# Performance work log

Hardware: AMD Instinct MI355X
Metric: run time of the kernel (lower is better)

## Reference

```python
import jax, jax.numpy as jnp
import numpy as np

HEAD = 8

def setup_inputs() -> dict:
    key = jax.random.key(0)
    ks = jax.random.split(key, 11)
    B, C, W, H = 16, 512, 32, 32
    d, N = C // HEAD, W * H
    return {
        "x": jax.random.normal(ks[0], (B, C, W, H), jnp.float32),
        "Wq": jax.random.normal(ks[1], (C, C), jnp.float32) * 0.02,
        "bq": jax.random.normal(ks[2], (C,), jnp.float32) * 0.02,
        "Wk": jax.random.normal(ks[3], (C, C), jnp.float32) * 0.02,
        "bk": jax.random.normal(ks[4], (C,), jnp.float32) * 0.02,
        "Wv": jax.random.normal(ks[5], (C, C), jnp.float32) * 0.02,
        "bv": jax.random.normal(ks[6], (C,), jnp.float32) * 0.02,
        "rel_h": jax.random.normal(ks[7], (1, HEAD, d, 1, H), jnp.float32),
        "rel_w": jax.random.normal(ks[8], (1, HEAD, d, W, 1), jnp.float32),
        "reg_qk": jax.random.normal(ks[9], (1, N, N), jnp.float32),
        "reg_v": jax.random.normal(ks[10], (1, d, N), jnp.float32),
    }

def reference(x, Wq, bq, Wk, bk, Wv, bv, rel_h, rel_w, reg_qk, reg_v):
    B, C, W, H = x.shape
    head = HEAD
    d = C // head
    N = W * H
    def conv1x1(inp, Wt, b):  # 1x1 conv == per-pixel linear
        return jnp.einsum('bchw,oc->bohw', inp, Wt) + b[None, :, None, None]
    q = conv1x1(x, Wq, bq).reshape(B, head, d, N)
    k = conv1x1(x, Wk, bk).reshape(B, head, d, N)
    v = conv1x1(x, Wv, bv).reshape(B, head, d, N)
    # content-content: q^T k -> [B, head, N, N]
    cc = jnp.einsum('bhdn,bhdm->bhnm', q, k)
    # content-position: (rel_h + rel_w) broadcast to [1, head, d, W, H] -> [head, N, d]
    pos = (rel_h + rel_w).reshape(head, d, N)
    cp = jnp.einsum('hdn,bhdm->bhnm', pos, q)
    energy = cc + cp  # [B, head, N, N]
    n_reg = reg_qk.shape[0]
    energy = jnp.concatenate(
        [energy, jnp.broadcast_to(reg_qk[None], (B, n_reg, N, N))], axis=1)
    v_all = jnp.concatenate(
        [v, jnp.broadcast_to(reg_v[None], (B, n_reg, d, N))], axis=1)
    attn = jax.nn.softmax(energy, axis=-1)  # [B, head+n_reg, N, N]
    # v @ attn^T
    out = jnp.einsum('bgdn,bgmn->bgdm', v_all, attn)
    out = out[:, :head].reshape(B, C, W, H)
    return out + x
```

## Files before the change

### kernel.cpp

```cpp
#include <hip/hip_runtime.h>

#define BB   16
#define HEADS 8
#define DH   64
#define NSP  1024
#define CCH  512

typedef unsigned int   u32;
typedef unsigned short u16;
typedef __attribute__((ext_vector_type(8))) short  short8;
typedef __attribute__((ext_vector_type(4))) float  floatx4;
typedef __attribute__((ext_vector_type(2))) unsigned uint2v;

#if defined(__has_builtin)
#if __has_builtin(__builtin_amdgcn_exp2f)
#define EXP2F(x) __builtin_amdgcn_exp2f(x)
#else
#define EXP2F(x) exp2f(x)
#endif
#if __has_builtin(__builtin_amdgcn_permlane32_swap)
#define HAVE_PL32 1
#endif
#if __has_builtin(__builtin_amdgcn_permlane16_swap)
#define HAVE_PL16 1
#endif
#else
#define EXP2F(x) exp2f(x)
#endif

__device__ __forceinline__ u16 f2b(float f) {
  u32 x = __float_as_uint(f);
  x = x + 0x7fffu + ((x >> 16) & 1u);
  return (u16)(x >> 16);
}

__device__ __forceinline__ u32 pkbf(float lo, float hi) {
  return __builtin_amdgcn_perm(__float_as_uint(hi) + 0x8000u,
                               __float_as_uint(lo) + 0x8000u, 0x07060302u);
}

__device__ __forceinline__ u32 pkcvt(float lo, float hi) {
  u32 d;
  asm("v_cvt_pk_bf16_f32 %0, %1, %2" : "=v"(d) : "v"(lo), "v"(hi));
  return d;
}

__device__ __forceinline__ void gload_lds16(const u16* g, u16* l) {
  __builtin_amdgcn_global_load_lds((const __attribute__((address_space(1))) u32*)g,
                                   (__attribute__((address_space(3))) u32*)l, 16, 0, 0);
}

__device__ __forceinline__ void lane32_swap(u32 a, u32 b, u32& ap, u32& bp, bool hi32) {
#ifdef HAVE_PL32
  uint2v r = __builtin_amdgcn_permlane32_swap(a, b, false, false);
  ap = r.x; bp = r.y;
  (void)hi32;
#else
  u32 sb = (u32)__shfl_xor((int)b, 32);
  u32 sa = (u32)__shfl_xor((int)a, 32);
  ap = hi32 ? sb : a;
  bp = hi32 ? b : sa;
#endif
}

__device__ __forceinline__ u32 lane16_xor(u32 x, bool qodd) {
#ifdef HAVE_PL16
  uint2v r = __builtin_amdgcn_permlane16_swap(x, x, false, false);
  return qodd ? r.x : r.y;
#else
  return (u32)__shfl_xor((int)x, 16);
#endif
}


__global__ __launch_bounds__(256) void prep_all(const float* __restrict__ x,
                                                const float* __restrict__ Wq,
                                                const float* __restrict__ Wk,
                                                const float* __restrict__ Wv,
                                                const float* __restrict__ rel_h,
                                                const float* __restrict__ rel_w,
                                                u16* __restrict__ wbf,
                                                u16* __restrict__ pos,
                                                u16* __restrict__ xt) {
  __shared__ float ld[64][68];
  int bid = blockIdx.x;
  int t = threadIdx.x;
  if (bid < 768) {
    int idx = bid * 256 + t;
    int which = idx >> 16;
    int r4 = (idx & 65535) * 4;
    const float* src = which == 0 ? Wq : which == 1 ? Wk : Wv;
    float4 v = *(const float4*)&src[r4];
    ushort4 s;
    s.x = f2b(v.x); s.y = f2b(v.y); s.z = f2b(v.z); s.w = f2b(v.w);
    *(ushort4*)&wbf[(which << 18) + r4] = s;
  } else if (bid < 2816) {
    int idx = (bid - 768) * 256 + t;
    int dd = idx & 63;
    int n  = (idx >> 6) & 1023;
    int hd = idx >> 16;
    int ww = n >> 5, hh = n & 31;
    float v = rel_h[(hd * 64 + dd) * 32 + hh] + rel_w[(hd * 64 + dd) * 32 + ww];
    int ntp = n >> 6, nbp = (n >> 4) & 3, rp = n & 15;
    int ksp = dd >> 5, qp = (dd >> 3) & 3, ep = dd & 7;
    size_t off = ((((size_t)(hd * 16 + ntp) * 4 + nbp) * 2 + ksp) * 64 + qp * 16 + rp) * 8 + ep;
    pos[off] = f2b(v);
  } else {
    int bid2 = bid - 2816;
    int ntile = bid2 & 15, ctile = (bid2 >> 4) & 7, b = bid2 >> 7;
    const float* xb = x + (((size_t)b * CCH + ctile * 64) << 10) + ntile * 64;
#pragma unroll
    for (int p = 0; p < 4; ++p) {
      int c = p * 16 + (t >> 4), n4 = (t & 15) * 4;
      float4 v = *(const float4*)&xb[((size_t)c << 10) + n4];
      ld[c][n4 + 0] = v.x; ld[c][n4 + 1] = v.y; ld[c][n4 + 2] = v.z; ld[c][n4 + 3] = v.w;
    }
    __syncthreads();
    u16* xo = xt + (((size_t)b << 10) + ntile * 64) * CCH + ctile * 64;
#pragma unroll
    for (int p = 0; p < 2; ++p) {
      int id = p * 256 + t;
      int n = id >> 3, c8 = (id & 7) * 8;
      ushort4 s0, s1;
      s0.x = f2b(ld[c8 + 0][n]); s0.y = f2b(ld[c8 + 1][n]);
      s0.z = f2b(ld[c8 + 2][n]); s0.w = f2b(ld[c8 + 3][n]);
      s1.x = f2b(ld[c8 + 4][n]); s1.y = f2b(ld[c8 + 5][n]);
      s1.z = f2b(ld[c8 + 6][n]); s1.w = f2b(ld[c8 + 7][n]);
      *(ushort4*)&xo[(size_t)n * CCH + c8] = s0;
      *(ushort4*)&xo[(size_t)n * CCH + c8 + 4] = s1;
    }
  }
}

__global__ __launch_bounds__(256, 2) void qkv_fused(const u16* __restrict__ wbf,
                                                    const u16* __restrict__ xt,
                                                    const float* __restrict__ bq,
                                                    const float* __restrict__ bk,
                                                    const float* __restrict__ bv,
                                                    u16* __restrict__ qw,
                                                    u16* __restrict__ kw,
                                                    u16* __restrict__ vtw) {
  int hid = blockIdx.x;
  int xcd  = hid & 7;
  int slot = hid >> 3;
  int otile = slot & 7;
  int pair  = xcd * 16 + (slot >> 3);
  int ntile = pair & 7;
  int b     = pair >> 3;
  int o0 = otile * 64, n0 = ntile * 128;

  __shared__ __align__(16) u16 smem[2 * 20480];

  int t = threadIdx.x;
  int w = t >> 6, lane = t & 63;
  int l15 = lane & 15, quad = lane >> 4;
  int srow = lane >> 3, sc = lane & 7;
  int scc = (sc ^ srow) << 3;

  floatx4 aq[8], ak[8], av[8];
#pragma unroll
  for (int i = 0; i < 8; ++i) {
    aq[i] = (floatx4){0.f, 0.f, 0.f, 0.f};
    ak[i] = (floatx4){0.f, 0.f, 0.f, 0.f};
    av[i] = (floatx4){0.f, 0.f, 0.f, 0.f};
  }

  auto stage = [&](int k0, int buf) {
    u16* base = smem + buf * 20480;
#pragma unroll
    for (int p = 0; p < 10; ++p) {
      int g0 = w * 80 + p * 8;
      if (g0 < 192) {
        int which = g0 >> 6;
        int r0 = g0 & 63;
        gload_lds16(wbf + ((size_t)which << 18) + (size_t)(o0 + r0 + srow) * CCH + k0 + scc,
                    base + which * 4096 + r0 * 64);
      } else {
        int r0 = g0 - 192;
        gload_lds16(xt + (size_t)(b * 1024 + n0 + r0 + srow) * CCH + k0 + scc,
                    base + 12288 + r0 * 64);
      }
    }
  };

  int rs = l15 & 7;
  int c0 = (quad ^ rs) << 3;
  int c1 = ((4 + quad) ^ rs) << 3;
  int wrow = (w * 16 + l15) * 64;

  stage(0, 0);
  stage(64, 1);

  for (int ki = 0; ki < 8; ++ki) {
    if (ki < 7) asm volatile("s_waitcnt vmcnt(10)" ::: "memory");
    else        asm volatile("s_waitcnt vmcnt(0)" ::: "memory");
    __builtin_amdgcn_s_barrier();
    __builtin_amdgcn_sched_barrier(0);

    u16* base = smem + (ki & 1) * 20480;
    u16* Xb = base + 12288;
#pragma unroll
    for (int ks = 0; ks < 2; ++ks) {
      int cc = ks ? c1 : c0;
      short8 fq = *(short8*)&base[wrow + cc];
      short8 fk = *(short8*)&base[4096 + wrow + cc];
      short8 fv = *(short8*)&base[8192 + wrow + cc];
#pragma unroll
      for (int ns = 0; ns < 8; ++ns) {
        short8 fx = *(short8*)&Xb[(ns * 16 + l15) * 64 + cc];
        aq[ns] = __builtin_amdgcn_mfma_f32_16x16x32_bf16(fq, fx, aq[ns], 0, 0, 0);
        ak[ns] = __builtin_amdgcn_mfma_f32_16x16x32_bf16(fk, fx, ak[ns], 0, 0, 0);
        av[ns] = __builtin_amdgcn_mfma_f32_16x16x32_bf16(fx, fv, av[ns], 0, 0, 0);
      }
    }

    if (ki < 6) {
      __builtin_amdgcn_sched_barrier(0);
      __builtin_amdgcn_s_barrier();
      stage((ki + 2) * 64, ki & 1);
    }
  }

  __syncthreads();
  u16* epQ = smem;
  u16* epK = smem + 9216;
  u16* epV = smem + 18432;
  {
    int ob = o0 + w * 16 + quad * 4;
    float q0 = bq[ob], q1 = bq[ob + 1], q2 = bq[ob + 2], q3 = bq[ob + 3];
    float k0b = bk[ob], k1b = bk[ob + 1], k2b = bk[ob + 2], k3b = bk[ob + 3];
    float vb = bv[o0 + w * 16 + l15];
#pragma unroll
    for (int ns = 0; ns < 8; ++ns) {
      int n = ns * 16 + l15;
      uint2 pk;
      pk.x = pkbf(aq[ns][0] + q0, aq[ns][1] + q1);
      pk.y = pkbf(aq[ns][2] + q2, aq[ns][3] + q3);
      *(uint2*)&epQ[n * 72 + w * 16 + quad * 4] = pk;
      pk.x = pkbf(ak[ns][0] + k0b, ak[ns][1] + k1b);
      pk.y = pkbf(ak[ns][2] + k2b, ak[ns][3] + k3b);
      *(uint2*)&epK[n * 72 + w * 16 + quad * 4] = pk;
      pk.x = pkbf(av[ns][0] + vb, av[ns][1] + vb);
      pk.y = pkbf(av[ns][2] + vb, av[ns][3] + vb);
      *(uint2*)&epV[(w * 16 + l15) * 136 + ns * 16 + quad * 4] = pk;
    }
  }
  __syncthreads();
  int h = otile;
  size_t bhI = (size_t)(b * HEADS + h);
  {
    int row = t >> 1, half = t & 1;
    int nt_ = (n0 + row) >> 6;
    int nblk_ = (row >> 4) & 3;
    int r_ = row & 15;
    size_t qkbase = (((bhI * 16 + nt_) * 4 + nblk_) * 2 + half) * 512;
#pragma unroll
    for (int i = 0; i < 4; ++i)
      *(uint4*)&qw[qkbase + (i * 16 + r_) * 8] = *(uint4*)&epQ[row * 72 + half * 32 + i * 8];
#pragma unroll
    for (int i = 0; i < 4; ++i)
      *(uint4*)&kw[qkbase + (i * 16 + r_) * 8] = *(uint4*)&epK[row * 72 + half * 32 + i * 8];
  }
  {
    int row = t >> 2, q4 = t & 3;
    int ddblk = row >> 4, r_ = row & 15;
#pragma unroll
    for (int i = 0; i < 4; ++i) {
      int nl = q4 * 32 + i * 8;
      int n = n0 + nl;
      int ntv = n >> 6, np = n & 63;
      int nh = np >> 5, q = (np >> 3) & 3;
      size_t vbase = (((bhI * 16 + ntv) * 4 + ddblk) * 2 + nh) * 512;
      *(uint4*)&vtw[vbase + (q * 16 + r_) * 8] = *(uint4*)&epV[row * 136 + nl];
    }
  }
}

__global__ __launch_bounds__(256, 2) void attn_mfma(const u16* __restrict__ qw,
                                                    const u16* __restrict__ kw,
                                                    const u16* __restrict__ vtw,
                                                    const u16* __restrict__ pos,
                                                    const float* __restrict__ x,
                                                    float* __restrict__ out) {
  int bh = blockIdx.x, mtile = blockIdx.y;
  int b = bh >> 3, h = bh & 7;
  __shared__ __align__(16) u16 smem_u16[36864];

  int t = threadIdx.x;
  int w = t >> 6, lane = t & 63;
  int l15 = lane & 15, quad = lane >> 4;
  bool qodd = (quad & 1) != 0;
  bool hi32 = lane >= 32;
  size_t bhs = (size_t)bh;
  int lane8 = lane * 8;

  short8 qa[4][2], pa[4][2];
  {
    const u16* qmb = qw + bhs * 65536 + (size_t)(mtile * 4 + w) * 4096;
    const u16* pmb = pos + (size_t)h * 65536 + (size_t)(mtile * 4 + w) * 4096;
#pragma unroll
    for (int msub = 0; msub < 4; ++msub)
#pragma unroll
      for (int ks = 0; ks < 2; ++ks) {
        int off = (msub * 2 + ks) * 512 + lane8;
        qa[msub][ks] = *(const short8*)(qmb + off);
        pa[msub][ks] = *(const short8*)(pmb + off);
      }
  }

  floatx4 oacc[4][4];
  float lsum[4] = {0.f, 0.f, 0.f, 0.f};
#pragma unroll
  for (int i = 0; i < 4; ++i)
#pragma unroll
    for (int j = 0; j < 4; ++j) oacc[i][j] = (floatx4){0.f, 0.f, 0.f, 0.f};

  const u16* kg = kw + bhs * 65536;
  const u16* qg = qw + bhs * 65536;
  const u16* vg = vtw + bhs * 65536;

  auto stage = [&](int nt, int buf) {
    u16* kt = smem_u16 + buf * 12288;
    u16* qt = kt + 4096;
    u16* vt = qt + 4096;
    const u16* kgt = kg + nt * 4096;
    const u16* qgt = qg + nt * 4096;
    const u16* vgt = vg + nt * 4096;
#pragma unroll
    for (int p = 0; p < 2; ++p) {
      int o = w * 1024 + p * 512;
      gload_lds16(kgt + o + lane8, kt + o);
      gload_lds16(qgt + o + lane8, qt + o);
      gload_lds16(vgt + o + lane8, vt + o);
    }
  };

  stage(0, 0);
  stage(1, 1);

  for (int nt = 0; nt < 16; ++nt) {
    __builtin_amdgcn_s_barrier();
    if (nt < 14) {
      stage(nt + 2, (nt + 2) % 3);
      asm volatile("s_waitcnt vmcnt(12)" ::: "memory");
    } else if (nt == 14) {
      asm volatile("s_waitcnt vmcnt(6)" ::: "memory");
    } else {
      asm volatile("s_waitcnt vmcnt(0)" ::: "memory");
    }
    __builtin_amdgcn_sched_barrier(0);

    u16* kt = smem_u16 + (nt % 3) * 12288;
    u16* qt = kt + 4096;
    u16* vt = qt + 4096;

#pragma unroll
    for (int half = 0; half < 2; ++half) {
      u32 Wd[4][4];
#pragma unroll
      for (int nblk2 = 0; nblk2 < 2; ++nblk2) {
        int nblk = half * 2 + nblk2;
        short8 kb0 = *(short8*)&kt[(nblk * 2 + 0) * 512 + lane8];
        short8 kb1 = *(short8*)&kt[(nblk * 2 + 1) * 512 + lane8];
        short8 qb0 = *(short8*)&qt[(nblk * 2 + 0) * 512 + lane8];
        short8 qb1 = *(short8*)&qt[(nblk * 2 + 1) * 512 + lane8];
        floatx4 sc4[4];
        __builtin_amdgcn_s_setprio(1);
#pragma unroll
        for (int msub = 0; msub < 4; ++msub) {
          floatx4 c = (floatx4){0.f, 0.f, 0.f, 0.f};
          c = __builtin_amdgcn_mfma_f32_16x16x32_bf16(kb0, qa[msub][0], c, 0, 0, 0);
          c = __builtin_amdgcn_mfma_f32_16x16x32_bf16(kb1, qa[msub][1], c, 0, 0, 0);
          c = __builtin_amdgcn_mfma_f32_16x16x32_bf16(qb0, pa[msub][0], c, 0, 0, 0);
          c = __builtin_amdgcn_mfma_f32_16x16x32_bf16(qb1, pa[msub][1], c, 0, 0, 0);
          sc4[msub] = c;
        }
        __builtin_amdgcn_s_setprio(0);
#pragma unroll
        for (int msub = 0; msub < 4; ++msub) {
          float p0 = EXP2F(fmaf(sc4[msub][0], 1.44269504f, -11.5415603f));
          float p1 = EXP2F(fmaf(sc4[msub][1], 1.44269504f, -11.5415603f));
          float p2 = EXP2F(fmaf(sc4[msub][2], 1.44269504f, -11.5415603f));
          float p3 = EXP2F(fmaf(sc4[msub][3], 1.44269504f, -11.5415603f));
          lsum[msub] += (p0 + p1) + (p2 + p3);
          Wd[msub][nblk2 * 2 + 0] = pkcvt(p0, p1);
          Wd[msub][nblk2 * 2 + 1] = pkcvt(p2, p3);
        }
      }
      short8 pB[4];
#pragma unroll
      for (int msub = 0; msub < 4; ++msub) {
        u32 A0p, B0p, A1p, B1p;
        lane32_swap(Wd[msub][0], Wd[msub][2], A0p, B0p, hi32);
        lane32_swap(Wd[msub][1], Wd[msub][3], A1p, B1p, hi32);
        u32 G0 = lane16_xor(qodd ? A0p : B0p, qodd);
        u32 G1 = lane16_xor(qodd ? A1p : B1p, qodd);
        union { u32 u[4]; short8 s; } cvt;
        cvt.u[0] = qodd ? G0 : A0p;
        cvt.u[1] = qodd ? G1 : A1p;
        cvt.u[2] = qodd ? B0p : G0;
        cvt.u[3] = qodd ? B1p : G1;
        pB[msub] = cvt.s;
      }
      __builtin_amdgcn_s_setprio(1);
#pragma unroll
      for (int dd = 0; dd < 4; ++dd) {
        short8 vb = *(short8*)&vt[(dd * 2 + half) * 512 + lane8];
#pragma unroll
        for (int msub = 0; msub < 4; ++msub)
          oacc[msub][dd] = __builtin_amdgcn_mfma_f32_16x16x32_bf16(vb, pB[msub], oacc[msub][dd], 0, 0, 0);
      }
      __builtin_amdgcn_s_setprio(0);
    }
  }

  float rinv[4];
#pragma unroll
  for (int msub = 0; msub < 4; ++msub) {
    float l = lsum[msub];
    l += __shfl_xor(l, 16);
    l += __shfl_xor(l, 32);
    rinv[msub] = 1.0f / l;
  }

  __syncthreads();
  float* ot = (float*)smem_u16 + w * 2304;
  int l8 = lane & 7, lr = lane >> 3;
#pragma unroll
  for (int mh = 0; mh < 2; ++mh) {
#pragma unroll
    for (int ms2 = 0; ms2 < 2; ++ms2) {
      int msub = mh * 2 + ms2;
#pragma unroll
      for (int dd = 0; dd < 4; ++dd)
#pragma unroll
        for (int r = 0; r < 4; ++r)
          ot[(dd * 16 + quad * 4 + r) * 36 + ms2 * 16 + l15] = oacc[msub][dd][r] * rinv[msub];
    }
#pragma unroll
    for (int pass = 0; pass < 8; ++pass) {
      int dd = pass * 8 + lr;
      float4 o4 = *(float4*)&ot[dd * 36 + l8 * 4];
      size_t off = (((size_t)b * CCH + h * DH + dd) << 10) + mtile * 256 + w * 64 + mh * 32 + l8 * 4;
      float4 xv = *(const float4*)&x[off];
      o4.x += xv.x; o4.y += xv.y; o4.z += xv.z; o4.w += xv.w;
      *(float4*)&out[off] = o4;
    }
  }
}

extern "C" void kernel_launch(void* const* d_in, const int* in_sizes, int n_in,
                              void* d_out, int out_size, void* d_ws, size_t ws_size,
                              hipStream_t stream) {
  const float* x     = (const float*)d_in[0];
  const float* Wq    = (const float*)d_in[1];
  const float* bq    = (const float*)d_in[2];
  const float* Wk    = (const float*)d_in[3];
  const float* bk    = (const float*)d_in[4];
  const float* Wv    = (const float*)d_in[5];
  const float* bv    = (const float*)d_in[6];
  const float* rel_h = (const float*)d_in[7];
  const float* rel_w = (const float*)d_in[8];
  float* out = (float*)d_out;

  char* ws = (char*)d_ws;
  u16* qw   = (u16*)(ws);
  u16* kw   = (u16*)(ws + ((size_t)16 << 20));
  u16* vtw  = (u16*)(ws + ((size_t)32 << 20));
  u16* pos  = (u16*)(ws + ((size_t)48 << 20));
  u16* wbf  = (u16*)(ws + ((size_t)49 << 20));
  u16* xt   = (u16*)d_out;

  hipLaunchKernelGGL(prep_all, dim3(4864), dim3(256), 0, stream,
                     x, Wq, Wk, Wv, rel_h, rel_w, wbf, pos, xt);
  hipLaunchKernelGGL(qkv_fused, dim3(1024), dim3(256), 0, stream,
                     wbf, xt, bq, bk, bv, qw, kw, vtw);
  hipLaunchKernelGGL(attn_mfma, dim3(128, 4), dim3(256), 0, stream,
                     qw, kw, vtw, pos, x, out);
}
```

Before: 192.6 us.

## Pre-swizzle QKV weights into fragment layout and load directly to registers

The weight conversion now writes bf16 weights in the per-lane MFMA fragment order, so qkv_fused loads weight fragments straight from global memory into registers (double-buffered across k-steps) instead of staging them through LDS. Only the x tile now goes through LDS, which cuts shared memory from 80KB to 32KB, and launch bounds are raised to 3 blocks per CU. The epilogue reuses one LDS buffer sequentially for Q, K and V, at the cost of extra barriers. The risks are more register pressure from the 12 held fragments, exposed global-load latency on the weights, and vmcnt wait counts that must still match the new load mix.

```diff
diff --git a/kernel.cpp b/kernel.cpp
--- a/kernel.cpp
+++ b/kernel.cpp
@@ -93,7 +93,12 @@
     float4 v = *(const float4*)&src[r4];
     ushort4 s;
     s.x = f2b(v.x); s.y = f2b(v.y); s.z = f2b(v.z); s.w = f2b(v.w);
-    *(ushort4*)&wbf[(which << 18) + r4] = s;
+    int o = r4 >> 9, c = r4 & 511;
+    int otile = o >> 6, w3 = (o >> 4) & 3, r = o & 15;
+    int ki = c >> 6, cl = c & 63, ks = cl >> 5, q = (cl >> 3) & 3, e = c & 7;
+    size_t off = ((((((size_t)which * 8 + otile) * 8 + ki) * 4 + w3) * 2 + ks) * 64
+                  + q * 16 + r) * 8 + e;
+    *(ushort4*)&wbf[off] = s;
   } else if (bid < 2816) {
     int idx = (bid - 768) * 256 + t;
     int dd = idx & 63;
@@ -132,7 +137,7 @@
   }
 }
 
-__global__ __launch_bounds__(256, 2) void qkv_fused(const u16* __restrict__ wbf,
+__global__ __launch_bounds__(256, 3) void qkv_fused(const u16* __restrict__ wbf,
                                                     const u16* __restrict__ xt,
                                                     const float* __restrict__ bq,
                                                     const float* __restrict__ bk,
@@ -149,13 +154,14 @@
   int b     = pair >> 3;
   int o0 = otile * 64, n0 = ntile * 128;
 
-  __shared__ __align__(16) u16 smem[2 * 20480];
+  __shared__ __align__(16) u16 smem[16384];
 
   int t = threadIdx.x;
   int w = t >> 6, lane = t & 63;
   int l15 = lane & 15, quad = lane >> 4;
   int srow = lane >> 3, sc = lane & 7;
   int scc = (sc ^ srow) << 3;
+  int lane8 = lane * 8;
 
   floatx4 aq[8], ak[8], av[8];
 #pragma unroll
@@ -166,45 +172,49 @@
   }
 
   auto stage = [&](int k0, int buf) {
-    u16* base = smem + buf * 20480;
-#pragma unroll
-    for (int p = 0; p < 10; ++p) {
-      int g0 = w * 80 + p * 8;
-      if (g0 < 192) {
-        int which = g0 >> 6;
-        int r0 = g0 & 63;
-        gload_lds16(wbf + ((size_t)which << 18) + (size_t)(o0 + r0 + srow) * CCH + k0 + scc,
-                    base + which * 4096 + r0 * 64);
-      } else {
-        int r0 = g0 - 192;
-        gload_lds16(xt + (size_t)(b * 1024 + n0 + r0 + srow) * CCH + k0 + scc,
-                    base + 12288 + r0 * 64);
-      }
-    }
+    u16* base = smem + buf * 8192;
+#pragma unroll
+    for (int p = 0; p < 4; ++p) {
+      int r0 = w * 32 + p * 8;
+      gload_lds16(xt + (size_t)(b * 1024 + n0 + r0 + srow) * CCH + k0 + scc,
+                  base + r0 * 64);
+    }
+  };
+
+  auto wfrag = [&](int which, int ki, int ks) {
+    size_t base = ((((((size_t)which * 8 + otile) * 8 + ki) * 4 + w) * 2 + ks) * 512);
+    return *(const short8*)&wbf[base + lane8];
   };
 
   int rs = l15 & 7;
   int c0 = (quad ^ rs) << 3;
   int c1 = ((4 + quad) ^ rs) << 3;
-  int wrow = (w * 16 + l15) * 64;
+
+  short8 Wf[2][6];
 
   stage(0, 0);
+#pragma unroll
+  for (int q_ = 0; q_ < 2; ++q_) {
+    Wf[0][0 * 2 + q_] = wfrag(0, 0, q_);
+    Wf[0][1 * 2 + q_] = wfrag(1, 0, q_);
+    Wf[0][2 * 2 + q_] = wfrag(2, 0, q_);
+  }
   stage(64, 1);
 
+#pragma unroll
   for (int ki = 0; ki < 8; ++ki) {
     if (ki < 7) asm volatile("s_waitcnt vmcnt(10)" ::: "memory");
-    else        asm volatile("s_waitcnt vmcnt(0)" ::: "memory");
+    else        asm volatile("s_waitcnt vmcnt(6)" ::: "memory");
     __builtin_amdgcn_s_barrier();
     __builtin_amdgcn_sched_barrier(0);
 
-    u16* base = smem + (ki & 1) * 20480;
-    u16* Xb = base + 12288;
+    u16* Xb = smem + (ki & 1) * 8192;
 #pragma unroll
     for (int ks = 0; ks < 2; ++ks) {
       int cc = ks ? c1 : c0;
-      short8 fq = *(short8*)&base[wrow + cc];
-      short8 fk = *(short8*)&base[4096 + wrow + cc];
-      short8 fv = *(short8*)&base[8192 + wrow + cc];
+      short8 fq = Wf[ki & 1][0 * 2 + ks];
+      short8 fk = Wf[ki & 1][1 * 2 + ks];
+      short8 fv = Wf[ki & 1][2 * 2 + ks];
 #pragma unroll
       for (int ns = 0; ns < 8; ++ns) {
         short8 fx = *(short8*)&Xb[(ns * 16 + l15) * 64 + cc];
@@ -214,40 +224,40 @@
       }
     }
 
+    if (ki < 7) {
+#pragma unroll
+      for (int q_ = 0; q_ < 2; ++q_) {
+        Wf[(ki + 1) & 1][0 * 2 + q_] = wfrag(0, ki + 1, q_);
+        Wf[(ki + 1) & 1][1 * 2 + q_] = wfrag(1, ki + 1, q_);
+        Wf[(ki + 1) & 1][2 * 2 + q_] = wfrag(2, ki + 1, q_);
+      }
+    }
+    __builtin_amdgcn_sched_barrier(0);
+
     if (ki < 6) {
-      __builtin_amdgcn_sched_barrier(0);
       __builtin_amdgcn_s_barrier();
       stage((ki + 2) * 64, ki & 1);
     }
   }
 
   __syncthreads();
-  u16* epQ = smem;
-  u16* epK = smem + 9216;
-  u16* epV = smem + 18432;
-  {
-    int ob = o0 + w * 16 + quad * 4;
+  u16* ep = smem;
+  int h = otile;
+  size_t bhI = (size_t)(b * HEADS + h);
+  int ob = o0 + w * 16 + quad * 4;
+
+  {
     float q0 = bq[ob], q1 = bq[ob + 1], q2 = bq[ob + 2], q3 = bq[ob + 3];
-    float k0b = bk[ob], k1b = bk[ob + 1], k2b = bk[ob + 2], k3b = bk[ob + 3];
-    float vb = bv[o0 + w * 16 + l15];
 #pragma unroll
     for (int ns = 0; ns < 8; ++ns) {
       int n = ns * 16 + l15;
       uint2 pk;
       pk.x = pkbf(aq[ns][0] + q0, aq[ns][1] + q1);
       pk.y = pkbf(aq[ns][2] + q2, aq[ns][3] + q3);
-      *(uint2*)&epQ[n * 72 + w * 16 + quad * 4] = pk;
-      pk.x = pkbf(ak[ns][0] + k0b, ak[ns][1] + k1b);
-      pk.y = pkbf(ak[ns][2] + k2b, ak[ns][3] + k3b);
-      *(uint2*)&epK[n * 72 + w * 16 + quad * 4] = pk;
-      pk.x = pkbf(av[ns][0] + vb, av[ns][1] + vb);
-      pk.y = pkbf(av[ns][2] + vb, av[ns][3] + vb);
-      *(uint2*)&epV[(w * 16 + l15) * 136 + ns * 16 + quad * 4] = pk;
-    }
-  }
-  __syncthreads();
-  int h = otile;
-  size_t bhI = (size_t)(b * HEADS + h);
+      *(uint2*)&ep[n * 72 + w * 16 + quad * 4] = pk;
+    }
+  }
+  __syncthreads();
   {
     int row = t >> 1, half = t & 1;
     int nt_ = (n0 + row) >> 6;
@@ -256,11 +266,45 @@
     size_t qkbase = (((bhI * 16 + nt_) * 4 + nblk_) * 2 + half) * 512;
 #pragma unroll
     for (int i = 0; i < 4; ++i)
-      *(uint4*)&qw[qkbase + (i * 16 + r_) * 8] = *(uint4*)&epQ[row * 72 + half * 32 + i * 8];
+      *(uint4*)&qw[qkbase + (i * 16 + r_) * 8] = *(uint4*)&ep[row * 72 + half * 32 + i * 8];
+  }
+  __syncthreads();
+
+  {
+    float k0b = bk[ob], k1b = bk[ob + 1], k2b = bk[ob + 2], k3b = bk[ob + 3];
+#pragma unroll
+    for (int ns = 0; ns < 8; ++ns) {
+      int n = ns * 16 + l15;
+      uint2 pk;
+      pk.x = pkbf(ak[ns][0] + k0b, ak[ns][1] + k1b);
+      pk.y = pkbf(ak[ns][2] + k2b, ak[ns][3] + k3b);
+      *(uint2*)&ep[n * 72 + w * 16 + quad * 4] = pk;
+    }
+  }
+  __syncthreads();
+  {
+    int row = t >> 1, half = t & 1;
+    int nt_ = (n0 + row) >> 6;
+    int nblk_ = (row >> 4) & 3;
+    int r_ = row & 15;
+    size_t qkbase = (((bhI * 16 + nt_) * 4 + nblk_) * 2 + half) * 512;
 #pragma unroll
     for (int i = 0; i < 4; ++i)
-      *(uint4*)&kw[qkbase + (i * 16 + r_) * 8] = *(uint4*)&epK[row * 72 + half * 32 + i * 8];
-  }
+      *(uint4*)&kw[qkbase + (i * 16 + r_) * 8] = *(uint4*)&ep[row * 72 + half * 32 + i * 8];
+  }
+  __syncthreads();
+
+  {
+    float vb = bv[o0 + w * 16 + l15];
+#pragma unroll
+    for (int ns = 0; ns < 8; ++ns) {
+      uint2 pk;
+      pk.x = pkbf(av[ns][0] + vb, av[ns][1] + vb);
+      pk.y = pkbf(av[ns][2] + vb, av[ns][3] + vb);
+      *(uint2*)&ep[(w * 16 + l15) * 136 + ns * 16 + quad * 4] = pk;
+    }
+  }
+  __syncthreads();
   {
     int row = t >> 2, q4 = t & 3;
     int ddblk = row >> 4, r_ = row & 15;
@@ -271,7 +315,7 @@
       int ntv = n >> 6, np = n & 63;
       int nh = np >> 5, q = (np >> 3) & 3;
       size_t vbase = (((bhI * 16 + ntv) * 4 + ddblk) * 2 + nh) * 512;
-      *(uint4*)&vtw[vbase + (q * 16 + r_) * 8] = *(uint4*)&epV[row * 136 + nl];
+      *(uint4*)&vtw[vbase + (q * 16 + r_) * 8] = *(uint4*)&ep[row * 136 + nl];
     }
   }
 }
```

Result: slower. 197.8 us (+2.7%).
